# Performance work log

Measured on AMD Instinct MI355X. Metric: run time of the kernel, lower is better.

Reference implementation:

```python
import jax, jax.numpy as jnp
import numpy as np

N, L, P = 1024, 4096, 8192  # batch, simulated length, acquired spectrum length


def batch_linspace(a, b, n):
    # a, b: [..., 1] -> [..., n]
    t = jnp.arange(n, dtype=jnp.float32) / (n - 1)
    return a + (b - a) * t


def bounded_random_walk(start, end, std, lower, upper, noise):
    """Vectorized bounded random walk with reflecting bounds.
    start/end/std/lower/upper: [N]; noise: [N, L] uniform(0,1) steps."""
    n = noise.shape[-1]
    rand = jnp.cumsum(std[:, None] * (noise - 0.5), axis=-1)          # [N, L]
    rand_trend = batch_linspace(rand[:, :1], rand[:, -1:], n)
    deltas = rand - rand_trend                                         # detrended walk
    bounds = (upper - lower)[:, None]
    span = deltas.max(-1, keepdims=True) - deltas.min(-1, keepdims=True)
    deltas = deltas / jnp.maximum(1.0, span / bounds)                  # squeeze into bound width
    trend = batch_linspace(start[:, None], end[:, None], n)
    ub = upper[:, None] - trend
    lb = lower[:, None] - trend
    over = deltas - ub
    deltas = jnp.where(over >= 0, ub - over, deltas)                   # reflect off upper bound
    under = lb - deltas
    deltas = jnp.where(under >= 0, lb + under, deltas)                 # reflect off lower bound
    return trend + deltas


def batch_smooth(x, w):
    """Per-sample box-filter smoothing with zero ('constant') padding.
    x: [N, L] float; w: [N] int window sizes."""
    n, l = x.shape
    xp = jnp.pad(x, ((0, 0), (l, l)))
    cs = jnp.concatenate([jnp.zeros((n, 1), x.dtype), jnp.cumsum(xp, -1)], -1)
    t = jnp.arange(l)
    lo = t[None, :] - w[:, None] // 2 + l                              # [N, L]
    hi = lo + w[:, None]
    box = jnp.take_along_axis(cs, hi, 1) - jnp.take_along_axis(cs, lo, 1)
    return box / w[:, None].astype(x.dtype)


def normalize_max(x):
    denom = jnp.max(jnp.abs(x), axis=-1, keepdims=True)
    return x / jnp.where(denom == 0, 1.0, denom)


def sim2acquired(sig, ppm_lo, ppm_hi, ppm):
    """Map simulated signal on [ppm_lo, ppm_hi] grid onto full acquired ppm axis
    (linear interp, zero outside simulated range)."""
    l = sig.shape[-1]
    xs = jnp.linspace(ppm_lo, ppm_hi, l)
    return jax.vmap(lambda s: jnp.interp(ppm, xs, s, left=0.0, right=0.0))(sig)


def hilbert(x):
    """FFT-based analytic signal; returns stacked [N, 2, P] (real, imag)."""
    p = x.shape[-1]
    h = jnp.zeros(p, x.dtype).at[0].set(1.0).at[p // 2].set(1.0).at[1:p // 2].set(2.0)
    a = jnp.fft.ifft(jnp.fft.fft(x, axis=-1) * h, axis=-1)
    return jnp.stack([jnp.real(a), jnp.imag(a)], axis=1)


def setup_inputs() -> dict:
    key = jax.random.key(0)
    ks = jax.random.split(key, 10)
    u = lambda k, lo, hi: jax.random.uniform(k, (N,), minval=lo, maxval=hi, dtype=jnp.float32)
    start = u(ks[0], -1.0, 1.0)
    end = u(ks[1], -1.0, 1.0)
    std = u(ks[2], 0.05, 0.3)
    lower_bnd = u(ks[3], -2.0, -1.5)
    upper_bnd = u(ks[4], 1.5, 2.0)
    windows = jax.random.randint(ks[5], (N,), 8, 128, dtype=jnp.int32)
    scale = u(ks[6], 0.5, 2.0)
    noise = jax.random.uniform(ks[7], (N, L), dtype=jnp.float32)
    omit_mask = (jax.random.uniform(ks[8], (N,)) > 0.1).astype(jnp.float32)  # drop_prob=0.1
    ppm = jnp.linspace(-2.0, 10.0, P).astype(jnp.float32)                     # acquired ppm axis
    ppm_range = jnp.array([0.2, 4.2], jnp.float32)                            # simulated range
    return dict(start=start, end=end, std=std, lower_bnd=lower_bnd,
                upper_bnd=upper_bnd, windows=windows, scale=scale, noise=noise,
                omit_mask=omit_mask, ppm=ppm, ppm_range=ppm_range)


def reference(start, end, std, lower_bnd, upper_bnd, windows, scale, noise,
              omit_mask, ppm, ppm_range):
    walk = bounded_random_walk(start, end, std, lower_bnd, upper_bnd, noise)  # [N, L]
    b = batch_smooth(walk, windows)
    trend = batch_linspace(b[:, :1], b[:, -1:], b.shape[-1])
    b = normalize_max(b - trend)
    b = b * omit_mask[:, None]                                                # rand_omit
    acq = sim2acquired(b * scale[:, None], ppm_range[0], ppm_range[1], ppm)   # [N, P]
    raw = hilbert(acq)                                                        # [N, 2, P]
    return (jnp.flip(raw, axis=-1), raw)
```

## Files before the change

### kernel.cpp

```cpp
#include <hip/hip_runtime.h>

#define NB 1024
#define LL 4096
#define PP 8192
#define FN 4096

#define PIF 3.14159265358979323846f

__device__ __forceinline__ float2 cadd(float2 a, float2 b){ return make_float2(a.x+b.x, a.y+b.y); }
__device__ __forceinline__ float2 csub(float2 a, float2 b){ return make_float2(a.x-b.x, a.y-b.y); }
__device__ __forceinline__ float2 cmul(float2 a, float2 b){ return make_float2(a.x*b.x - a.y*b.y, a.x*b.y + a.y*b.x); }

__device__ __forceinline__ int SW(int p){ return p ^ ((p >> 4) & 15); }

__device__ __forceinline__ int rho(int k){
    return ((k & 3) << 10) | (((k >> 2) & 3) << 8) | (((k >> 4) & 3) << 6)
         | (((k >> 6) & 3) << 4) | (((k >> 8) & 3) << 2) | ((k >> 10) & 3);
}

template<int H>
__device__ __forceinline__ void fwd_r4(float2* buf, int tid){
#pragma unroll
    for (int m = 0; m < FN/4/256; m++){
        int b = tid + m*256;
        int j = b & (H-1);
        int i = ((b & ~(H-1)) << 2) | j;
        int a0 = SW(i), a1 = SW(i+H), a2 = SW(i+2*H), a3 = SW(i+3*H);
        float2 x0 = buf[a0], x1 = buf[a1], x2 = buf[a2], x3 = buf[a3];
        float2 t0 = cadd(x0,x2), t1 = cadd(x1,x3);
        float2 t2 = csub(x0,x2), t3 = csub(x1,x3);
        float2 y0 = cadd(t0,t1);
        float2 y2 = csub(t0,t1);
        float2 y1 = make_float2(t2.x + t3.y, t2.y - t3.x);
        float2 y3 = make_float2(t2.x - t3.y, t2.y + t3.x);
        if (H > 1){
            float sn, cn; __sincosf((-PIF/(2.0f*(float)H)) * (float)j, &sn, &cn);
            float2 E  = make_float2(cn, sn);
            float2 E2 = cmul(E,E);
            float2 E3 = cmul(E2,E);
            y1 = cmul(y1,E); y2 = cmul(y2,E2); y3 = cmul(y3,E3);
        }
        buf[a0] = y0; buf[a1] = y1; buf[a2] = y2; buf[a3] = y3;
    }
}

template<int H>
__device__ __forceinline__ void inv_r4(float2* buf, int tid){
#pragma unroll
    for (int m = 0; m < FN/4/256; m++){
        int b = tid + m*256;
        int j = b & (H-1);
        int i = ((b & ~(H-1)) << 2) | j;
        int a0 = SW(i), a1 = SW(i+H), a2 = SW(i+2*H), a3 = SW(i+3*H);
        float2 z0 = buf[a0], z1 = buf[a1], z2 = buf[a2], z3 = buf[a3];
        if (H > 1){
            float sn, cn; __sincosf((PIF/(2.0f*(float)H)) * (float)j, &sn, &cn);
            float2 E  = make_float2(cn, sn);
            float2 E2 = cmul(E,E);
            float2 E3 = cmul(E2,E);
            z1 = cmul(z1,E); z2 = cmul(z2,E2); z3 = cmul(z3,E3);
        }
        float2 s0 = cadd(z0,z2), s1 = cadd(z1,z3);
        float2 s2 = csub(z0,z2), s3 = csub(z1,z3);
        buf[a0] = cadd(s0,s1);
        buf[a2] = csub(s0,s1);
        buf[a1] = make_float2(s2.x - s3.y, s2.y + s3.x);
        buf[a3] = make_float2(s2.x + s3.y, s2.y - s3.x);
    }
}

__device__ __forceinline__ void hilbert_mid(float2* buf, int tid){
    const float s = 1.0f/(2.0f*(float)FN);
#pragma unroll
    for (int m = 0; m < 8; m++){
        int k = ((tid & 31) << 6) | ((tid >> 5) << 3) | m;
        if (k == 0){
            buf[0] = make_float2(0.0f, 0.0f);
            int p = SW(2);
            float2 Z = buf[p];
            buf[p] = make_float2(-2.0f*s*Z.y, 2.0f*s*Z.x);
        } else {
            int pk = SW(rho(k));
            int pj = SW(rho(FN - k));
            float2 Zk = buf[pk];
            float2 Zj = buf[pj];
            float ux = Zk.x + Zj.x, uy = Zk.y - Zj.y;
            float vx = Zk.x - Zj.x, vy = Zk.y + Zj.y;
            float sn, cn; __sincosf((PIF/(float)FN) * (float)k, &sn, &cn);
            float2 zk, zj;
            zk.x = s * ((ux*cn - uy*sn) - (vx*cn + vy*sn));
            zk.y = s * ((ux*sn + uy*cn) + (vx*sn - vy*cn));
            float u2x = ux,  u2y = -uy;
            float v2x = -vx, v2y = vy;
            zj.x = s * ((v2x*cn - v2y*sn) - (u2x*cn + u2y*sn));
            zj.y = s * ((v2x*sn + v2y*cn) + (u2x*sn - u2y*cn));
            buf[pk] = zk;
            buf[pj] = zj;
        }
    }
}

__global__ __launch_bounds__(256, 4) void k_all(
    const float* __restrict__ g_start,
    const float* __restrict__ g_end,
    const float* __restrict__ g_std,
    const float* __restrict__ g_low,
    const float* __restrict__ g_up,
    const int*   __restrict__ g_win,
    const float* __restrict__ g_scale,
    const float* __restrict__ g_noise,
    const float* __restrict__ g_omit,
    const float* __restrict__ g_ppm,
    const float* __restrict__ g_ppmr,
    float* __restrict__ g_out)
{
    __shared__ float2 buf[FN];
    float* bf  = (float*)buf;
#define CSI(t) ((t) + ((t) >> 5))
    float* cs  = bf;
    float* tmp = bf + 4226;
    float* shv = bf + 4234;

    const int n    = blockIdx.x;
    const int tid  = threadIdx.x;
    const int lane = tid & 63;
    const int wid  = tid >> 6;
    const float st = g_start[n];
    const float en = g_end[n];
    const float sd = g_std[n];
    const float lo = g_low[n];
    const float up = g_up[n];
    const int   w  = g_win[n];
    const float inv_nm1 = 1.0f / (float)(LL - 1);

    float v[16];
    {
        const float4* p = (const float4*)(g_noise + (size_t)n * LL) + (size_t)tid * 4;
#pragma unroll
        for (int q = 0; q < 4; q++) {
            float4 t4 = p[q];
            v[4*q+0] = t4.x; v[4*q+1] = t4.y; v[4*q+2] = t4.z; v[4*q+3] = t4.w;
        }
    }
#pragma unroll
    for (int k = 0; k < 16; k++) v[k] = sd * (v[k] - 0.5f);

    float run = 0.0f;
#pragma unroll
    for (int k = 0; k < 16; k++) { run += v[k]; v[k] = run; }
    float ws = run;
#pragma unroll
    for (int off = 1; off < 64; off <<= 1) { float t = __shfl_up(ws, off); if (lane >= off) ws += t; }
    if (lane == 63) tmp[wid] = ws;
    if (tid == 0)   shv[0] = v[0];
    __syncthreads();
    float w0 = tmp[0], w1 = tmp[1], w2s = tmp[2], w3 = tmp[3];
    const float rT = w0 + w1 + w2s + w3;
    const float r0 = shv[0];
    float base = (wid > 0 ? w0 : 0.0f) + (wid > 1 ? w1 : 0.0f) + (wid > 2 ? w2s : 0.0f);
    float excl = base + ws - run;
    __syncthreads();

    float del[16];
    float mx = -INFINITY, mn = INFINITY;
#pragma unroll
    for (int k = 0; k < 16; k++) {
        int t = tid * 16 + k;
        float d = (excl + v[k]) - (r0 + (rT - r0) * ((float)t * inv_nm1));
        del[k] = d;
        mx = fmaxf(mx, d); mn = fminf(mn, d);
    }
#pragma unroll
    for (int off = 32; off > 0; off >>= 1) {
        mx = fmaxf(mx, __shfl_xor(mx, off));
        mn = fminf(mn, __shfl_xor(mn, off));
    }
    if (lane == 0) { tmp[wid] = mx; tmp[4 + wid] = mn; }
    __syncthreads();
    mx = fmaxf(fmaxf(tmp[0], tmp[1]), fmaxf(tmp[2], tmp[3]));
    mn = fminf(fminf(tmp[4], tmp[5]), fminf(tmp[6], tmp[7]));
    __syncthreads();

    const float qs = fmaxf(1.0f, (mx - mn) / (up - lo));

    float wv[16];
#pragma unroll
    for (int k = 0; k < 16; k++) {
        int t = tid * 16 + k;
        float tr  = st + (en - st) * ((float)t * inv_nm1);
        float ub  = up - tr;
        float lb2 = lo - tr;
        float d = del[k] / qs;
        float over = d - ub;
        d = (over >= 0.0f) ? (ub - over) : d;
        float under = lb2 - d;
        d = (under >= 0.0f) ? (lb2 + under) : d;
        wv[k] = tr + d;
    }

    run = 0.0f;
#pragma unroll
    for (int k = 0; k < 16; k++) { run += wv[k]; wv[k] = run; }
    ws = run;
#pragma unroll
    for (int off = 1; off < 64; off <<= 1) { float t = __shfl_up(ws, off); if (lane >= off) ws += t; }
    if (lane == 63) tmp[wid] = ws;
    __syncthreads();
    w0 = tmp[0]; w1 = tmp[1]; w2s = tmp[2]; w3 = tmp[3];
    const float grand2 = w0 + w1 + w2s + w3;
    base = (wid > 0 ? w0 : 0.0f) + (wid > 1 ? w1 : 0.0f) + (wid > 2 ? w2s : 0.0f);
    float excl2 = base + ws - run;
#pragma unroll
    for (int k = 0; k < 16; k++) {
        int t = tid * 16 + k;
        cs[CSI(t)] = excl2 + ((k == 0) ? 0.0f : wv[k - 1]);
    }
    if (tid == 255) cs[CSI(LL)] = grand2;
    __syncthreads();

    const int wh = w / 2;
    const float invw = 1.0f / (float)w;
    float bvals[16];
#pragma unroll
    for (int k = 0; k < 16; k++) {
        int t  = tid + 256 * k;
        int li = t - wh;
        int hi = li + w;
        li = (li < 0) ? 0 : li;
        hi = (hi > LL) ? LL : hi;
        bvals[k] = (cs[CSI(hi)] - cs[CSI(li)]) * invw;
    }
    if (tid == 0)   shv[0] = bvals[0];
    if (tid == 255) shv[1] = bvals[15];
    __syncthreads();
    const float b0 = shv[0], bL = shv[1];

    float am = 0.0f;
#pragma unroll
    for (int k = 0; k < 16; k++) {
        int t = tid + 256 * k;
        bvals[k] -= b0 + (bL - b0) * ((float)t * inv_nm1);
        am = fmaxf(am, fabsf(bvals[k]));
    }
#pragma unroll
    for (int off = 32; off > 0; off >>= 1) am = fmaxf(am, __shfl_xor(am, off));
    if (lane == 0) tmp[wid] = am;
    __syncthreads();
    float denom = fmaxf(fmaxf(tmp[0], tmp[1]), fmaxf(tmp[2], tmp[3]));
    denom = (denom == 0.0f) ? 1.0f : denom;
    const float fac = g_omit[n] * g_scale[n] / denom;

#pragma unroll
    for (int k = 0; k < 16; k++) {
        int t = tid + 256 * k;
        bf[t] = bvals[k] * fac;
    }
    __syncthreads();

    const float xlo = g_ppmr[0];
    const float xhi = g_ppmr[1];
    const float posmul = (float)(LL - 1) / (xhi - xlo);
    float val[PP / 256];
#pragma unroll
    for (int m = 0; m < PP / 256; m++) {
        int jj = tid + m * 256;
        float x = g_ppm[jj];
        float re = 0.0f;
        if (x >= xlo && x <= xhi) {
            float pos = (x - xlo) * posmul;
            int idx = (int)floorf(pos);
            idx = (idx < 0) ? 0 : ((idx > LL - 2) ? (LL - 2) : idx);
            float fr = pos - (float)idx;
            float s0 = bf[idx], s1 = bf[idx + 1];
            re = s0 + (s1 - s0) * fr;
        }
        val[m] = re;
    }
    __syncthreads();

    const size_t base1 = (size_t)NB * 2 * PP + (size_t)n * 2 * PP;
    const size_t base0 = (size_t)n * 2 * PP;
#pragma unroll
    for (int m = 0; m < PP / 256; m++) {
        int jj = tid + m * 256;
        bf[2 * SW(jj >> 1) + (jj & 1)] = val[m];
        g_out[base1 + jj]            = val[m];
        g_out[base0 + (PP - 1 - jj)] = val[m];
    }
    __syncthreads();

    fwd_r4<1024>(buf, tid); __syncthreads();
    fwd_r4< 256>(buf, tid); __syncthreads();
    fwd_r4<  64>(buf, tid); __syncthreads();
    fwd_r4<  16>(buf, tid); __syncthreads();
    fwd_r4<   4>(buf, tid); __syncthreads();
    fwd_r4<   1>(buf, tid); __syncthreads();

    hilbert_mid(buf, tid); __syncthreads();

    inv_r4<   1>(buf, tid); __syncthreads();
    inv_r4<   4>(buf, tid); __syncthreads();
    inv_r4<  16>(buf, tid); __syncthreads();
    inv_r4<  64>(buf, tid); __syncthreads();
    inv_r4< 256>(buf, tid); __syncthreads();
    inv_r4<1024>(buf, tid); __syncthreads();

#pragma unroll
    for (int m = 0; m < FN / 256; m++) {
        int p = tid + m * 256;
        float2 a = buf[SW(p)];
        *(float2*)(g_out + base1 + PP + 2 * p)          = a;
        *(float2*)(g_out + base0 + 2 * PP - 2 - 2 * p)  = make_float2(a.y, a.x);
    }
}

extern "C" void kernel_launch(void* const* d_in, const int* in_sizes, int n_in,
                              void* d_out, int out_size, void* d_ws, size_t ws_size,
                              hipStream_t stream)
{
    const float* start = (const float*)d_in[0];
    const float* end_  = (const float*)d_in[1];
    const float* stdv  = (const float*)d_in[2];
    const float* lowb  = (const float*)d_in[3];
    const float* upb   = (const float*)d_in[4];
    const int*   win   = (const int*)d_in[5];
    const float* scl   = (const float*)d_in[6];
    const float* noise = (const float*)d_in[7];
    const float* omit  = (const float*)d_in[8];
    const float* ppm   = (const float*)d_in[9];
    const float* ppmr  = (const float*)d_in[10];
    float* out = (float*)d_out;

    hipLaunchKernelGGL(k_all, dim3(NB), dim3(256), 0, stream,
                       start, end_, stdv, lowb, upb, win, scl, noise, omit,
                       ppm, ppmr, out);
}
```

Before: 187.4 us.

## Fuse FFT radix-4 stages into register-resident radix-16 passes

Replaces the six-pass radix-4 shared-memory FFT (and its inverse) with three passes that each do two radix-4 stages on 16 values held in registers. Interpolation results feed the first pass directly from registers, and the last inverse pass writes straight to global memory. This removes several LDS round-trips and barriers per transform and uses vectorized float2 loads and stores for ppm and outputs. The cost is higher register pressure from the 16-element complex arrays, which may reduce occupancy.

```diff
diff --git a/kernel.cpp b/kernel.cpp
--- a/kernel.cpp
+++ b/kernel.cpp
@@ -18,55 +18,52 @@
          | (((k >> 6) & 3) << 4) | (((k >> 8) & 3) << 2) | ((k >> 10) & 3);
 }
 
-template<int H>
-__device__ __forceinline__ void fwd_r4(float2* buf, int tid){
-#pragma unroll
-    for (int m = 0; m < FN/4/256; m++){
-        int b = tid + m*256;
-        int j = b & (H-1);
-        int i = ((b & ~(H-1)) << 2) | j;
-        int a0 = SW(i), a1 = SW(i+H), a2 = SW(i+2*H), a3 = SW(i+3*H);
-        float2 x0 = buf[a0], x1 = buf[a1], x2 = buf[a2], x3 = buf[a3];
-        float2 t0 = cadd(x0,x2), t1 = cadd(x1,x3);
-        float2 t2 = csub(x0,x2), t3 = csub(x1,x3);
-        float2 y0 = cadd(t0,t1);
-        float2 y2 = csub(t0,t1);
-        float2 y1 = make_float2(t2.x + t3.y, t2.y - t3.x);
-        float2 y3 = make_float2(t2.x - t3.y, t2.y + t3.x);
-        if (H > 1){
-            float sn, cn; __sincosf((-PIF/(2.0f*(float)H)) * (float)j, &sn, &cn);
-            float2 E  = make_float2(cn, sn);
-            float2 E2 = cmul(E,E);
-            float2 E3 = cmul(E2,E);
-            y1 = cmul(y1,E); y2 = cmul(y2,E2); y3 = cmul(y3,E3);
-        }
-        buf[a0] = y0; buf[a1] = y1; buf[a2] = y2; buf[a3] = y3;
-    }
-}
-
-template<int H>
-__device__ __forceinline__ void inv_r4(float2* buf, int tid){
-#pragma unroll
-    for (int m = 0; m < FN/4/256; m++){
-        int b = tid + m*256;
-        int j = b & (H-1);
-        int i = ((b & ~(H-1)) << 2) | j;
-        int a0 = SW(i), a1 = SW(i+H), a2 = SW(i+2*H), a3 = SW(i+3*H);
-        float2 z0 = buf[a0], z1 = buf[a1], z2 = buf[a2], z3 = buf[a3];
-        if (H > 1){
-            float sn, cn; __sincosf((PIF/(2.0f*(float)H)) * (float)j, &sn, &cn);
-            float2 E  = make_float2(cn, sn);
-            float2 E2 = cmul(E,E);
-            float2 E3 = cmul(E2,E);
-            z1 = cmul(z1,E); z2 = cmul(z2,E2); z3 = cmul(z3,E3);
-        }
-        float2 s0 = cadd(z0,z2), s1 = cadd(z1,z3);
-        float2 s2 = csub(z0,z2), s3 = csub(z1,z3);
-        buf[a0] = cadd(s0,s1);
-        buf[a2] = csub(s0,s1);
-        buf[a1] = make_float2(s2.x - s3.y, s2.y + s3.x);
-        buf[a3] = make_float2(s2.x + s3.y, s2.y - s3.x);
-    }
+__device__ __forceinline__ float2 CFc(int a){
+    return (a==1) ? make_float2(0.92387953251f, -0.38268343236f)
+         : (a==2) ? make_float2(0.70710678119f, -0.70710678119f)
+         :          make_float2(0.38268343236f, -0.92387953251f);
+}
+__device__ __forceinline__ float2 CIc(int a){ float2 c = CFc(a); return make_float2(c.x, -c.y); }
+
+template<int S>
+__device__ __forceinline__ void bf4f(float2* x, float2 E){
+    float2 E2 = cmul(E,E), E3 = cmul(E2,E);
+    float2 t0 = cadd(x[0],x[2*S]), t1 = cadd(x[S],x[3*S]);
+    float2 t2 = csub(x[0],x[2*S]), t3 = csub(x[S],x[3*S]);
+    x[0]   = cadd(t0,t1);
+    x[2*S] = cmul(csub(t0,t1), E2);
+    x[S]   = cmul(make_float2(t2.x + t3.y, t2.y - t3.x), E);
+    x[3*S] = cmul(make_float2(t2.x - t3.y, t2.y + t3.x), E3);
+}
+template<int S>
+__device__ __forceinline__ void bf4f_nt(float2* x){
+    float2 t0 = cadd(x[0],x[2*S]), t1 = cadd(x[S],x[3*S]);
+    float2 t2 = csub(x[0],x[2*S]), t3 = csub(x[S],x[3*S]);
+    x[0]   = cadd(t0,t1);
+    x[2*S] = csub(t0,t1);
+    x[S]   = make_float2(t2.x + t3.y, t2.y - t3.x);
+    x[3*S] = make_float2(t2.x - t3.y, t2.y + t3.x);
+}
+template<int S>
+__device__ __forceinline__ void bf4i(float2* x, float2 E){
+    float2 E2 = cmul(E,E), E3 = cmul(E2,E);
+    float2 z0 = x[0], z1 = cmul(x[S],E), z2 = cmul(x[2*S],E2), z3 = cmul(x[3*S],E3);
+    float2 s0 = cadd(z0,z2), s1 = cadd(z1,z3);
+    float2 s2 = csub(z0,z2), s3 = csub(z1,z3);
+    x[0]   = cadd(s0,s1);
+    x[2*S] = csub(s0,s1);
+    x[S]   = make_float2(s2.x - s3.y, s2.y + s3.x);
+    x[3*S] = make_float2(s2.x + s3.y, s2.y - s3.x);
+}
+template<int S>
+__device__ __forceinline__ void bf4i_nt(float2* x){
+    float2 z0 = x[0], z1 = x[S], z2 = x[2*S], z3 = x[3*S];
+    float2 s0 = cadd(z0,z2), s1 = cadd(z1,z3);
+    float2 s2 = csub(z0,z2), s3 = csub(z1,z3);
+    x[0]   = cadd(s0,s1);
+    x[2*S] = csub(s0,s1);
+    x[S]   = make_float2(s2.x - s3.y, s2.y + s3.x);
+    x[3*S] = make_float2(s2.x + s3.y, s2.y - s3.x);
 }
 
 __device__ __forceinline__ void hilbert_mid(float2* buf, int tid){
@@ -260,57 +257,166 @@
     const float xlo = g_ppmr[0];
     const float xhi = g_ppmr[1];
     const float posmul = (float)(LL - 1) / (xhi - xlo);
-    float val[PP / 256];
-#pragma unroll
-    for (int m = 0; m < PP / 256; m++) {
-        int jj = tid + m * 256;
-        float x = g_ppm[jj];
-        float re = 0.0f;
-        if (x >= xlo && x <= xhi) {
-            float pos = (x - xlo) * posmul;
-            int idx = (int)floorf(pos);
-            idx = (idx < 0) ? 0 : ((idx > LL - 2) ? (LL - 2) : idx);
-            float fr = pos - (float)idx;
-            float s0 = bf[idx], s1 = bf[idx + 1];
-            re = s0 + (s1 - s0) * fr;
-        }
-        val[m] = re;
-    }
-    __syncthreads();
-
     const size_t base1 = (size_t)NB * 2 * PP + (size_t)n * 2 * PP;
     const size_t base0 = (size_t)n * 2 * PP;
-#pragma unroll
-    for (int m = 0; m < PP / 256; m++) {
-        int jj = tid + m * 256;
-        bf[2 * SW(jj >> 1) + (jj & 1)] = val[m];
-        g_out[base1 + jj]            = val[m];
-        g_out[base0 + (PP - 1 - jj)] = val[m];
-    }
-    __syncthreads();
-
-    fwd_r4<1024>(buf, tid); __syncthreads();
-    fwd_r4< 256>(buf, tid); __syncthreads();
-    fwd_r4<  64>(buf, tid); __syncthreads();
-    fwd_r4<  16>(buf, tid); __syncthreads();
-    fwd_r4<   4>(buf, tid); __syncthreads();
-    fwd_r4<   1>(buf, tid); __syncthreads();
-
-    hilbert_mid(buf, tid); __syncthreads();
-
-    inv_r4<   1>(buf, tid); __syncthreads();
-    inv_r4<   4>(buf, tid); __syncthreads();
-    inv_r4<  16>(buf, tid); __syncthreads();
-    inv_r4<  64>(buf, tid); __syncthreads();
-    inv_r4< 256>(buf, tid); __syncthreads();
-    inv_r4<1024>(buf, tid); __syncthreads();
-
-#pragma unroll
-    for (int m = 0; m < FN / 256; m++) {
-        int p = tid + m * 256;
-        float2 a = buf[SW(p)];
-        *(float2*)(g_out + base1 + PP + 2 * p)          = a;
-        *(float2*)(g_out + base0 + 2 * PP - 2 - 2 * p)  = make_float2(a.y, a.x);
+
+    auto interp1 = [&](float x) -> float {
+        if (x < xlo || x > xhi) return 0.0f;
+        float pos = (x - xlo) * posmul;
+        int idx = (int)floorf(pos);
+        idx = (idx < 0) ? 0 : ((idx > LL - 2) ? (LL - 2) : idx);
+        float fr = pos - (float)idx;
+        float s0 = bf[idx], s1 = bf[idx + 1];
+        return s0 + (s1 - s0) * fr;
+    };
+
+    float2 X[16];
+#pragma unroll
+    for (int b = 0; b < 4; b++)
+#pragma unroll
+    for (int a = 0; a < 4; a++) {
+        int p = tid + 256 * a + 1024 * b;
+        float2 pm = *(const float2*)(g_ppm + 2 * p);
+        float re0 = interp1(pm.x);
+        float re1 = interp1(pm.y);
+        X[a + 4 * b] = make_float2(re0, re1);
+        *(float2*)(g_out + base1 + 2 * p)          = make_float2(re0, re1);
+        *(float2*)(g_out + base0 + PP - 2 - 2 * p) = make_float2(re1, re0);
+    }
+    __syncthreads();
+
+    {
+        float sn, cn;
+        __sincosf((-PIF / 2048.0f) * (float)tid, &sn, &cn);
+        float2 Eb = make_float2(cn, sn);
+#pragma unroll
+        for (int a = 0; a < 4; a++) {
+            float2 E = (a == 0) ? Eb : cmul(Eb, CFc(a));
+            bf4f<4>(&X[a], E);
+        }
+        __sincosf((-PIF / 512.0f) * (float)tid, &sn, &cn);
+        float2 E = make_float2(cn, sn);
+#pragma unroll
+        for (int b = 0; b < 4; b++) bf4f<1>(&X[4 * b], E);
+#pragma unroll
+        for (int b = 0; b < 4; b++)
+#pragma unroll
+        for (int a = 0; a < 4; a++)
+            buf[SW(tid + 256 * a + 1024 * b)] = X[a + 4 * b];
+    }
+    __syncthreads();
+
+    const int u  = tid >> 4;
+    const int lw = tid & 15;
+    const int pb = u * 256 + lw;
+    {
+#pragma unroll
+        for (int b = 0; b < 4; b++)
+#pragma unroll
+        for (int a = 0; a < 4; a++)
+            X[a + 4 * b] = buf[SW(pb + 64 * b + 16 * a)];
+        float sn, cn;
+        __sincosf((-PIF / 128.0f) * (float)lw, &sn, &cn);
+        float2 Eb = make_float2(cn, sn);
+#pragma unroll
+        for (int a = 0; a < 4; a++) {
+            float2 E = (a == 0) ? Eb : cmul(Eb, CFc(a));
+            bf4f<4>(&X[a], E);
+        }
+        __sincosf((-PIF / 32.0f) * (float)lw, &sn, &cn);
+        float2 E = make_float2(cn, sn);
+#pragma unroll
+        for (int b = 0; b < 4; b++) bf4f<1>(&X[4 * b], E);
+#pragma unroll
+        for (int b = 0; b < 4; b++)
+#pragma unroll
+        for (int a = 0; a < 4; a++)
+            buf[SW(pb + 64 * b + 16 * a)] = X[a + 4 * b];
+    }
+    __syncthreads();
+
+    {
+#pragma unroll
+        for (int c = 0; c < 16; c++) X[c] = buf[SW(16 * tid + c)];
+        bf4f_nt<4>(&X[0]);
+#pragma unroll
+        for (int a = 1; a < 4; a++) bf4f<4>(&X[a], CFc(a));
+#pragma unroll
+        for (int b = 0; b < 4; b++) bf4f_nt<1>(&X[4 * b]);
+#pragma unroll
+        for (int c = 0; c < 16; c++) buf[SW(16 * tid + c)] = X[c];
+    }
+    __syncthreads();
+
+    hilbert_mid(buf, tid);
+    __syncthreads();
+
+    {
+#pragma unroll
+        for (int c = 0; c < 16; c++) X[c] = buf[SW(16 * tid + c)];
+#pragma unroll
+        for (int b = 0; b < 4; b++) bf4i_nt<1>(&X[4 * b]);
+        bf4i_nt<4>(&X[0]);
+#pragma unroll
+        for (int a = 1; a < 4; a++) bf4i<4>(&X[a], CIc(a));
+#pragma unroll
+        for (int c = 0; c < 16; c++) buf[SW(16 * tid + c)] = X[c];
+    }
+    __syncthreads();
+
+    {
+#pragma unroll
+        for (int b = 0; b < 4; b++)
+#pragma unroll
+        for (int a = 0; a < 4; a++)
+            X[a + 4 * b] = buf[SW(pb + 64 * b + 16 * a)];
+        float sn, cn;
+        __sincosf((PIF / 32.0f) * (float)lw, &sn, &cn);
+        float2 E = make_float2(cn, sn);
+#pragma unroll
+        for (int b = 0; b < 4; b++) bf4i<1>(&X[4 * b], E);
+        __sincosf((PIF / 128.0f) * (float)lw, &sn, &cn);
+        float2 Eb = make_float2(cn, sn);
+#pragma unroll
+        for (int a = 0; a < 4; a++) {
+            float2 Ea = (a == 0) ? Eb : cmul(Eb, CIc(a));
+            bf4i<4>(&X[a], Ea);
+        }
+#pragma unroll
+        for (int b = 0; b < 4; b++)
+#pragma unroll
+        for (int a = 0; a < 4; a++)
+            buf[SW(pb + 64 * b + 16 * a)] = X[a + 4 * b];
+    }
+    __syncthreads();
+
+    {
+#pragma unroll
+        for (int b = 0; b < 4; b++)
+#pragma unroll
+        for (int a = 0; a < 4; a++)
+            X[a + 4 * b] = buf[SW(tid + 256 * a + 1024 * b)];
+        float sn, cn;
+        __sincosf((PIF / 512.0f) * (float)tid, &sn, &cn);
+        float2 E = make_float2(cn, sn);
+#pragma unroll
+        for (int b = 0; b < 4; b++) bf4i<1>(&X[4 * b], E);
+        __sincosf((PIF / 2048.0f) * (float)tid, &sn, &cn);
+        float2 Eb = make_float2(cn, sn);
+#pragma unroll
+        for (int a = 0; a < 4; a++) {
+            float2 Ea = (a == 0) ? Eb : cmul(Eb, CIc(a));
+            bf4i<4>(&X[a], Ea);
+        }
+#pragma unroll
+        for (int b = 0; b < 4; b++)
+#pragma unroll
+        for (int a = 0; a < 4; a++) {
+            int p = tid + 256 * a + 1024 * b;
+            float2 vv = X[a + 4 * b];
+            *(float2*)(g_out + base1 + PP + 2 * p)         = vv;
+            *(float2*)(g_out + base0 + 2 * PP - 2 - 2 * p) = make_float2(vv.y, vv.x);
+        }
     }
 }
 
```

New measurement: 188.5 us. No clear change (+0.6%).

## Switch Hilbert FFT to radix-8 register stages with 512-thread blocks

Applied to the files above, without the earlier changes.

Replaces the six radix-4 shared-memory FFT passes (each way) with four radix-8 passes, where the first forward pass and last inverse pass run directly on register data. This removes one shared-memory round trip and a barrier per direction. Block size doubles to 512 threads with 8 elements per thread, and the padded shared layout changes from an XOR swizzle to a +2-per-16 pad. The interp and output stores are also vectorized as float2. Risks are higher register pressure and a larger shared footprint that may limit occupancy.

```diff
diff --git a/kernel.cpp b/kernel.cpp
--- a/kernel.cpp
+++ b/kernel.cpp
@@ -11,96 +11,46 @@
 __device__ __forceinline__ float2 csub(float2 a, float2 b){ return make_float2(a.x-b.x, a.y-b.y); }
 __device__ __forceinline__ float2 cmul(float2 a, float2 b){ return make_float2(a.x*b.x - a.y*b.y, a.x*b.y + a.y*b.x); }
 
-__device__ __forceinline__ int SW(int p){ return p ^ ((p >> 4) & 15); }
-
-__device__ __forceinline__ int rho(int k){
-    return ((k & 3) << 10) | (((k >> 2) & 3) << 8) | (((k >> 4) & 3) << 6)
-         | (((k >> 6) & 3) << 4) | (((k >> 8) & 3) << 2) | ((k >> 10) & 3);
+__device__ __forceinline__ int PH2(int p){ return p + 2*(p >> 4); }
+
+__device__ __forceinline__ int rev8(int k){
+    return ((k & 7) << 9) | (((k >> 3) & 7) << 6) | (((k >> 6) & 7) << 3) | ((k >> 9) & 7);
 }
 
-template<int H>
-__device__ __forceinline__ void fwd_r4(float2* buf, int tid){
-#pragma unroll
-    for (int m = 0; m < FN/4/256; m++){
-        int b = tid + m*256;
-        int j = b & (H-1);
-        int i = ((b & ~(H-1)) << 2) | j;
-        int a0 = SW(i), a1 = SW(i+H), a2 = SW(i+2*H), a3 = SW(i+3*H);
-        float2 x0 = buf[a0], x1 = buf[a1], x2 = buf[a2], x3 = buf[a3];
-        float2 t0 = cadd(x0,x2), t1 = cadd(x1,x3);
-        float2 t2 = csub(x0,x2), t3 = csub(x1,x3);
-        float2 y0 = cadd(t0,t1);
-        float2 y2 = csub(t0,t1);
-        float2 y1 = make_float2(t2.x + t3.y, t2.y - t3.x);
-        float2 y3 = make_float2(t2.x - t3.y, t2.y + t3.x);
-        if (H > 1){
-            float sn, cn; __sincosf((-PIF/(2.0f*(float)H)) * (float)j, &sn, &cn);
-            float2 E  = make_float2(cn, sn);
-            float2 E2 = cmul(E,E);
-            float2 E3 = cmul(E2,E);
-            y1 = cmul(y1,E); y2 = cmul(y2,E2); y3 = cmul(y3,E3);
-        }
-        buf[a0] = y0; buf[a1] = y1; buf[a2] = y2; buf[a3] = y3;
-    }
+__device__ __forceinline__ void core8f(float2* x){
+    const float c8 = 0.70710678118654752f;
+    float2 e0=cadd(x[0],x[4]), e1=cadd(x[1],x[5]), e2=cadd(x[2],x[6]), e3=cadd(x[3],x[7]);
+    float2 o0=csub(x[0],x[4]), o1=csub(x[1],x[5]), o2=csub(x[2],x[6]), o3=csub(x[3],x[7]);
+    float2 t1 = make_float2(c8*(o1.x + o1.y), c8*(o1.y - o1.x));
+    float2 t2 = make_float2(o2.y, -o2.x);
+    float2 t3 = make_float2(c8*(o3.y - o3.x), -c8*(o3.x + o3.y));
+    float2 a0=cadd(e0,e2), a1=cadd(e1,e3), a2=csub(e0,e2), a3=csub(e1,e3);
+    x[0]=cadd(a0,a1); x[4]=csub(a0,a1);
+    x[2]=make_float2(a2.x + a3.y, a2.y - a3.x);
+    x[6]=make_float2(a2.x - a3.y, a2.y + a3.x);
+    float2 b0=cadd(o0,t2), b1=cadd(t1,t3), b2=csub(o0,t2), b3=csub(t1,t3);
+    x[1]=cadd(b0,b1); x[5]=csub(b0,b1);
+    x[3]=make_float2(b2.x + b3.y, b2.y - b3.x);
+    x[7]=make_float2(b2.x - b3.y, b2.y + b3.x);
 }
-
-template<int H>
-__device__ __forceinline__ void inv_r4(float2* buf, int tid){
-#pragma unroll
-    for (int m = 0; m < FN/4/256; m++){
-        int b = tid + m*256;
-        int j = b & (H-1);
-        int i = ((b & ~(H-1)) << 2) | j;
-        int a0 = SW(i), a1 = SW(i+H), a2 = SW(i+2*H), a3 = SW(i+3*H);
-        float2 z0 = buf[a0], z1 = buf[a1], z2 = buf[a2], z3 = buf[a3];
-        if (H > 1){
-            float sn, cn; __sincosf((PIF/(2.0f*(float)H)) * (float)j, &sn, &cn);
-            float2 E  = make_float2(cn, sn);
-            float2 E2 = cmul(E,E);
-            float2 E3 = cmul(E2,E);
-            z1 = cmul(z1,E); z2 = cmul(z2,E2); z3 = cmul(z3,E3);
-        }
-        float2 s0 = cadd(z0,z2), s1 = cadd(z1,z3);
-        float2 s2 = csub(z0,z2), s3 = csub(z1,z3);
-        buf[a0] = cadd(s0,s1);
-        buf[a2] = csub(s0,s1);
-        buf[a1] = make_float2(s2.x - s3.y, s2.y + s3.x);
-        buf[a3] = make_float2(s2.x + s3.y, s2.y - s3.x);
-    }
+__device__ __forceinline__ void core8i(float2* x){
+    const float c8 = 0.70710678118654752f;
+    float2 e0=cadd(x[0],x[4]), e1=cadd(x[1],x[5]), e2=cadd(x[2],x[6]), e3=cadd(x[3],x[7]);
+    float2 o0=csub(x[0],x[4]), o1=csub(x[1],x[5]), o2=csub(x[2],x[6]), o3=csub(x[3],x[7]);
+    float2 t1 = make_float2(c8*(o1.x - o1.y), c8*(o1.y + o1.x));
+    float2 t2 = make_float2(-o2.y, o2.x);
+    float2 t3 = make_float2(-c8*(o3.x + o3.y), c8*(o3.x - o3.y));
+    float2 a0=cadd(e0,e2), a1=cadd(e1,e3), a2=csub(e0,e2), a3=csub(e1,e3);
+    x[0]=cadd(a0,a1); x[4]=csub(a0,a1);
+    x[2]=make_float2(a2.x - a3.y, a2.y + a3.x);
+    x[6]=make_float2(a2.x + a3.y, a2.y - a3.x);
+    float2 b0=cadd(o0,t2), b1=cadd(t1,t3), b2=csub(o0,t2), b3=csub(t1,t3);
+    x[1]=cadd(b0,b1); x[5]=csub(b0,b1);
+    x[3]=make_float2(b2.x - b3.y, b2.y + b3.x);
+    x[7]=make_float2(b2.x + b3.y, b2.y - b3.x);
 }
 
-__device__ __forceinline__ void hilbert_mid(float2* buf, int tid){
-    const float s = 1.0f/(2.0f*(float)FN);
-#pragma unroll
-    for (int m = 0; m < 8; m++){
-        int k = ((tid & 31) << 6) | ((tid >> 5) << 3) | m;
-        if (k == 0){
-            buf[0] = make_float2(0.0f, 0.0f);
-            int p = SW(2);
-            float2 Z = buf[p];
-            buf[p] = make_float2(-2.0f*s*Z.y, 2.0f*s*Z.x);
-        } else {
-            int pk = SW(rho(k));
-            int pj = SW(rho(FN - k));
-            float2 Zk = buf[pk];
-            float2 Zj = buf[pj];
-            float ux = Zk.x + Zj.x, uy = Zk.y - Zj.y;
-            float vx = Zk.x - Zj.x, vy = Zk.y + Zj.y;
-            float sn, cn; __sincosf((PIF/(float)FN) * (float)k, &sn, &cn);
-            float2 zk, zj;
-            zk.x = s * ((ux*cn - uy*sn) - (vx*cn + vy*sn));
-            zk.y = s * ((ux*sn + uy*cn) + (vx*sn - vy*cn));
-            float u2x = ux,  u2y = -uy;
-            float v2x = -vx, v2y = vy;
-            zj.x = s * ((v2x*cn - v2y*sn) - (u2x*cn + u2y*sn));
-            zj.y = s * ((v2x*sn + v2y*cn) + (u2x*sn - u2y*cn));
-            buf[pk] = zk;
-            buf[pj] = zj;
-        }
-    }
-}
-
-__global__ __launch_bounds__(256, 4) void k_all(
+__global__ __launch_bounds__(512, 6) void k_all(
     const float* __restrict__ g_start,
     const float* __restrict__ g_end,
     const float* __restrict__ g_std,
@@ -114,12 +64,12 @@
     const float* __restrict__ g_ppmr,
     float* __restrict__ g_out)
 {
-    __shared__ float2 buf[FN];
+    __shared__ alignas(16) float2 buf[4608];
     float* bf  = (float*)buf;
 #define CSI(t) ((t) + ((t) >> 5))
     float* cs  = bf;
     float* tmp = bf + 4226;
-    float* shv = bf + 4234;
+    float* shv = bf + 4242;
 
     const int n    = blockIdx.x;
     const int tid  = threadIdx.x;
@@ -133,41 +83,39 @@
     const int   w  = g_win[n];
     const float inv_nm1 = 1.0f / (float)(LL - 1);
 
-    float v[16];
-    {
-        const float4* p = (const float4*)(g_noise + (size_t)n * LL) + (size_t)tid * 4;
-#pragma unroll
-        for (int q = 0; q < 4; q++) {
-            float4 t4 = p[q];
-            v[4*q+0] = t4.x; v[4*q+1] = t4.y; v[4*q+2] = t4.z; v[4*q+3] = t4.w;
-        }
-    }
-#pragma unroll
-    for (int k = 0; k < 16; k++) v[k] = sd * (v[k] - 0.5f);
+    float r[8];
+    {
+        const float4* p = (const float4*)(g_noise + (size_t)n * LL) + (size_t)tid * 2;
+        float4 ta = p[0], tb = p[1];
+        r[0]=ta.x; r[1]=ta.y; r[2]=ta.z; r[3]=ta.w;
+        r[4]=tb.x; r[5]=tb.y; r[6]=tb.z; r[7]=tb.w;
+    }
+#pragma unroll
+    for (int k = 0; k < 8; k++) r[k] = sd * (r[k] - 0.5f);
 
     float run = 0.0f;
 #pragma unroll
-    for (int k = 0; k < 16; k++) { run += v[k]; v[k] = run; }
+    for (int k = 0; k < 8; k++) { run += r[k]; r[k] = run; }
     float ws = run;
 #pragma unroll
     for (int off = 1; off < 64; off <<= 1) { float t = __shfl_up(ws, off); if (lane >= off) ws += t; }
     if (lane == 63) tmp[wid] = ws;
-    if (tid == 0)   shv[0] = v[0];
-    __syncthreads();
-    float w0 = tmp[0], w1 = tmp[1], w2s = tmp[2], w3 = tmp[3];
-    const float rT = w0 + w1 + w2s + w3;
+    if (tid == 0)   shv[0] = r[0];
+    __syncthreads();
+    float t0=tmp[0],t1=tmp[1],t2=tmp[2],t3=tmp[3],t4=tmp[4],t5=tmp[5],t6=tmp[6],t7=tmp[7];
+    const float rT = ((t0+t1)+(t2+t3))+((t4+t5)+(t6+t7));
     const float r0 = shv[0];
-    float base = (wid > 0 ? w0 : 0.0f) + (wid > 1 ? w1 : 0.0f) + (wid > 2 ? w2s : 0.0f);
+    float base = (wid>0?t0:0.f)+(wid>1?t1:0.f)+(wid>2?t2:0.f)+(wid>3?t3:0.f)
+               + (wid>4?t4:0.f)+(wid>5?t5:0.f)+(wid>6?t6:0.f);
     float excl = base + ws - run;
     __syncthreads();
 
-    float del[16];
     float mx = -INFINITY, mn = INFINITY;
 #pragma unroll
-    for (int k = 0; k < 16; k++) {
-        int t = tid * 16 + k;
-        float d = (excl + v[k]) - (r0 + (rT - r0) * ((float)t * inv_nm1));
-        del[k] = d;
+    for (int k = 0; k < 8; k++) {
+        int t = tid * 8 + k;
+        float d = (excl + r[k]) - (r0 + (rT - r0) * ((float)t * inv_nm1));
+        r[k] = d;
         mx = fmaxf(mx, d); mn = fminf(mn, d);
     }
 #pragma unroll
@@ -175,142 +123,291 @@
         mx = fmaxf(mx, __shfl_xor(mx, off));
         mn = fminf(mn, __shfl_xor(mn, off));
     }
-    if (lane == 0) { tmp[wid] = mx; tmp[4 + wid] = mn; }
-    __syncthreads();
-    mx = fmaxf(fmaxf(tmp[0], tmp[1]), fmaxf(tmp[2], tmp[3]));
-    mn = fminf(fminf(tmp[4], tmp[5]), fminf(tmp[6], tmp[7]));
+    if (lane == 0) { tmp[wid] = mx; tmp[8 + wid] = mn; }
+    __syncthreads();
+    mx = fmaxf(fmaxf(fmaxf(tmp[0],tmp[1]),fmaxf(tmp[2],tmp[3])),
+               fmaxf(fmaxf(tmp[4],tmp[5]),fmaxf(tmp[6],tmp[7])));
+    mn = fminf(fminf(fminf(tmp[8],tmp[9]),fminf(tmp[10],tmp[11])),
+               fminf(fminf(tmp[12],tmp[13]),fminf(tmp[14],tmp[15])));
     __syncthreads();
 
     const float qs = fmaxf(1.0f, (mx - mn) / (up - lo));
 
-    float wv[16];
-#pragma unroll
-    for (int k = 0; k < 16; k++) {
-        int t = tid * 16 + k;
+#pragma unroll
+    for (int k = 0; k < 8; k++) {
+        int t = tid * 8 + k;
         float tr  = st + (en - st) * ((float)t * inv_nm1);
         float ub  = up - tr;
         float lb2 = lo - tr;
-        float d = del[k] / qs;
+        float d = r[k] / qs;
         float over = d - ub;
         d = (over >= 0.0f) ? (ub - over) : d;
         float under = lb2 - d;
         d = (under >= 0.0f) ? (lb2 + under) : d;
-        wv[k] = tr + d;
+        r[k] = tr + d;
     }
 
     run = 0.0f;
 #pragma unroll
-    for (int k = 0; k < 16; k++) { run += wv[k]; wv[k] = run; }
+    for (int k = 0; k < 8; k++) { run += r[k]; r[k] = run; }
     ws = run;
 #pragma unroll
     for (int off = 1; off < 64; off <<= 1) { float t = __shfl_up(ws, off); if (lane >= off) ws += t; }
     if (lane == 63) tmp[wid] = ws;
     __syncthreads();
-    w0 = tmp[0]; w1 = tmp[1]; w2s = tmp[2]; w3 = tmp[3];
-    const float grand2 = w0 + w1 + w2s + w3;
-    base = (wid > 0 ? w0 : 0.0f) + (wid > 1 ? w1 : 0.0f) + (wid > 2 ? w2s : 0.0f);
+    t0=tmp[0];t1=tmp[1];t2=tmp[2];t3=tmp[3];t4=tmp[4];t5=tmp[5];t6=tmp[6];t7=tmp[7];
+    const float grand2 = ((t0+t1)+(t2+t3))+((t4+t5)+(t6+t7));
+    base = (wid>0?t0:0.f)+(wid>1?t1:0.f)+(wid>2?t2:0.f)+(wid>3?t3:0.f)
+         + (wid>4?t4:0.f)+(wid>5?t5:0.f)+(wid>6?t6:0.f);
     float excl2 = base + ws - run;
 #pragma unroll
-    for (int k = 0; k < 16; k++) {
-        int t = tid * 16 + k;
-        cs[CSI(t)] = excl2 + ((k == 0) ? 0.0f : wv[k - 1]);
-    }
-    if (tid == 255) cs[CSI(LL)] = grand2;
+    for (int k = 0; k < 8; k++) {
+        int t = tid * 8 + k;
+        cs[CSI(t)] = excl2 + ((k == 0) ? 0.0f : r[k - 1]);
+    }
+    if (tid == 511) cs[CSI(LL)] = grand2;
     __syncthreads();
 
     const int wh = w / 2;
     const float invw = 1.0f / (float)w;
-    float bvals[16];
-#pragma unroll
-    for (int k = 0; k < 16; k++) {
-        int t  = tid + 256 * k;
+#pragma unroll
+    for (int k = 0; k < 8; k++) {
+        int t  = tid + 512 * k;
         int li = t - wh;
         int hi = li + w;
         li = (li < 0) ? 0 : li;
         hi = (hi > LL) ? LL : hi;
-        bvals[k] = (cs[CSI(hi)] - cs[CSI(li)]) * invw;
-    }
-    if (tid == 0)   shv[0] = bvals[0];
-    if (tid == 255) shv[1] = bvals[15];
+        r[k] = (cs[CSI(hi)] - cs[CSI(li)]) * invw;
+    }
+    if (tid == 0)   shv[0] = r[0];
+    if (tid == 511) shv[1] = r[7];
     __syncthreads();
     const float b0 = shv[0], bL = shv[1];
 
     float am = 0.0f;
 #pragma unroll
-    for (int k = 0; k < 16; k++) {
-        int t = tid + 256 * k;
-        bvals[k] -= b0 + (bL - b0) * ((float)t * inv_nm1);
-        am = fmaxf(am, fabsf(bvals[k]));
+    for (int k = 0; k < 8; k++) {
+        int t = tid + 512 * k;
+        r[k] -= b0 + (bL - b0) * ((float)t * inv_nm1);
+        am = fmaxf(am, fabsf(r[k]));
     }
 #pragma unroll
     for (int off = 32; off > 0; off >>= 1) am = fmaxf(am, __shfl_xor(am, off));
     if (lane == 0) tmp[wid] = am;
     __syncthreads();
-    float denom = fmaxf(fmaxf(tmp[0], tmp[1]), fmaxf(tmp[2], tmp[3]));
+    float denom = fmaxf(fmaxf(fmaxf(tmp[0],tmp[1]),fmaxf(tmp[2],tmp[3])),
+                        fmaxf(fmaxf(tmp[4],tmp[5]),fmaxf(tmp[6],tmp[7])));
     denom = (denom == 0.0f) ? 1.0f : denom;
     const float fac = g_omit[n] * g_scale[n] / denom;
-
-#pragma unroll
-    for (int k = 0; k < 16; k++) {
-        int t = tid + 256 * k;
-        bf[t] = bvals[k] * fac;
+    __syncthreads();
+
+#pragma unroll
+    for (int k = 0; k < 8; k++) {
+        int t = tid + 512 * k;
+        bf[t] = r[k] * fac;
     }
     __syncthreads();
 
     const float xlo = g_ppmr[0];
     const float xhi = g_ppmr[1];
     const float posmul = (float)(LL - 1) / (xhi - xlo);
-    float val[PP / 256];
-#pragma unroll
-    for (int m = 0; m < PP / 256; m++) {
-        int jj = tid + m * 256;
-        float x = g_ppm[jj];
-        float re = 0.0f;
-        if (x >= xlo && x <= xhi) {
-            float pos = (x - xlo) * posmul;
-            int idx = (int)floorf(pos);
-            idx = (idx < 0) ? 0 : ((idx > LL - 2) ? (LL - 2) : idx);
-            float fr = pos - (float)idx;
-            float s0 = bf[idx], s1 = bf[idx + 1];
-            re = s0 + (s1 - s0) * fr;
-        }
-        val[m] = re;
-    }
-    __syncthreads();
-
     const size_t base1 = (size_t)NB * 2 * PP + (size_t)n * 2 * PP;
     const size_t base0 = (size_t)n * 2 * PP;
-#pragma unroll
-    for (int m = 0; m < PP / 256; m++) {
-        int jj = tid + m * 256;
-        bf[2 * SW(jj >> 1) + (jj & 1)] = val[m];
-        g_out[base1 + jj]            = val[m];
-        g_out[base0 + (PP - 1 - jj)] = val[m];
-    }
-    __syncthreads();
-
-    fwd_r4<1024>(buf, tid); __syncthreads();
-    fwd_r4< 256>(buf, tid); __syncthreads();
-    fwd_r4<  64>(buf, tid); __syncthreads();
-    fwd_r4<  16>(buf, tid); __syncthreads();
-    fwd_r4<   4>(buf, tid); __syncthreads();
-    fwd_r4<   1>(buf, tid); __syncthreads();
-
-    hilbert_mid(buf, tid); __syncthreads();
-
-    inv_r4<   1>(buf, tid); __syncthreads();
-    inv_r4<   4>(buf, tid); __syncthreads();
-    inv_r4<  16>(buf, tid); __syncthreads();
-    inv_r4<  64>(buf, tid); __syncthreads();
-    inv_r4< 256>(buf, tid); __syncthreads();
-    inv_r4<1024>(buf, tid); __syncthreads();
-
-#pragma unroll
-    for (int m = 0; m < FN / 256; m++) {
-        int p = tid + m * 256;
-        float2 a = buf[SW(p)];
-        *(float2*)(g_out + base1 + PP + 2 * p)          = a;
-        *(float2*)(g_out + base0 + 2 * PP - 2 - 2 * p)  = make_float2(a.y, a.x);
+
+    auto interp1 = [&](float x) -> float {
+        if (x < xlo || x > xhi) return 0.0f;
+        float pos = (x - xlo) * posmul;
+        int idx = (int)floorf(pos);
+        idx = (idx < 0) ? 0 : ((idx > LL - 2) ? (LL - 2) : idx);
+        float fr = pos - (float)idx;
+        float s0 = bf[idx], s1 = bf[idx + 1];
+        return s0 + (s1 - s0) * fr;
+    };
+
+    float2 X[8];
+#pragma unroll
+    for (int m = 0; m < 8; m++) {
+        int p = tid + 512 * m;
+        float2 pm = *(const float2*)(g_ppm + 2 * p);
+        float re0 = interp1(pm.x);
+        float re1 = interp1(pm.y);
+        X[m] = make_float2(re0, re1);
+        *(float2*)(g_out + base1 + 2 * p)          = make_float2(re0, re1);
+        *(float2*)(g_out + base0 + PP - 2 - 2 * p) = make_float2(re1, re0);
+    }
+    __syncthreads();
+
+    const int bA = tid + 2 * (tid >> 4);
+    {
+        core8f(X);
+        float sn, cn; __sincosf((-PIF / 2048.0f) * (float)tid, &sn, &cn);
+        float2 E = make_float2(cn, sn), Er = E;
+        buf[bA]        = X[0];
+        buf[bA +  576] = cmul(X[1], Er); Er = cmul(Er, E);
+        buf[bA + 1152] = cmul(X[2], Er); Er = cmul(Er, E);
+        buf[bA + 1728] = cmul(X[3], Er); Er = cmul(Er, E);
+        buf[bA + 2304] = cmul(X[4], Er); Er = cmul(Er, E);
+        buf[bA + 2880] = cmul(X[5], Er); Er = cmul(Er, E);
+        buf[bA + 3456] = cmul(X[6], Er); Er = cmul(Er, E);
+        buf[bA + 4032] = cmul(X[7], Er);
+    }
+    __syncthreads();
+
+    const int j2 = tid & 63;
+    const int bB = (tid >> 6) * 576 + j2 + 2 * (j2 >> 4);
+    {
+#pragma unroll
+        for (int d = 0; d < 8; d++) X[d] = buf[bB + 72 * d];
+        core8f(X);
+        float sn, cn; __sincosf((-PIF / 256.0f) * (float)j2, &sn, &cn);
+        float2 E = make_float2(cn, sn), Er = E;
+        buf[bB]       = X[0];
+        buf[bB +  72] = cmul(X[1], Er); Er = cmul(Er, E);
+        buf[bB + 144] = cmul(X[2], Er); Er = cmul(Er, E);
+        buf[bB + 216] = cmul(X[3], Er); Er = cmul(Er, E);
+        buf[bB + 288] = cmul(X[4], Er); Er = cmul(Er, E);
+        buf[bB + 360] = cmul(X[5], Er); Er = cmul(Er, E);
+        buf[bB + 432] = cmul(X[6], Er); Er = cmul(Er, E);
+        buf[bB + 504] = cmul(X[7], Er);
+    }
+    __syncthreads();
+
+    const int j3 = tid & 7;
+    const int bC = (tid >> 3) * 72 + j3;
+    {
+        X[0]=buf[bC];    X[1]=buf[bC+8];  X[2]=buf[bC+18]; X[3]=buf[bC+26];
+        X[4]=buf[bC+36]; X[5]=buf[bC+44]; X[6]=buf[bC+54]; X[7]=buf[bC+62];
+        core8f(X);
+        float sn, cn; __sincosf((-PIF / 32.0f) * (float)j3, &sn, &cn);
+        float2 E = make_float2(cn, sn), Er = E;
+        buf[bC]    = X[0];
+        buf[bC+ 8] = cmul(X[1], Er); Er = cmul(Er, E);
+        buf[bC+18] = cmul(X[2], Er); Er = cmul(Er, E);
+        buf[bC+26] = cmul(X[3], Er); Er = cmul(Er, E);
+        buf[bC+36] = cmul(X[4], Er); Er = cmul(Er, E);
+        buf[bC+44] = cmul(X[5], Er); Er = cmul(Er, E);
+        buf[bC+54] = cmul(X[6], Er); Er = cmul(Er, E);
+        buf[bC+62] = cmul(X[7], Er);
+    }
+    __syncthreads();
+
+    const int f4 = 4 * tid + (tid >> 1);
+    float4* b4 = reinterpret_cast<float4*>(buf);
+    {
+        float4 a0 = b4[f4], a1 = b4[f4+1], a2 = b4[f4+2], a3 = b4[f4+3];
+        X[0]=make_float2(a0.x,a0.y); X[1]=make_float2(a0.z,a0.w);
+        X[2]=make_float2(a1.x,a1.y); X[3]=make_float2(a1.z,a1.w);
+        X[4]=make_float2(a2.x,a2.y); X[5]=make_float2(a2.z,a2.w);
+        X[6]=make_float2(a3.x,a3.y); X[7]=make_float2(a3.z,a3.w);
+        core8f(X);
+        b4[f4]   = make_float4(X[0].x,X[0].y,X[1].x,X[1].y);
+        b4[f4+1] = make_float4(X[2].x,X[2].y,X[3].x,X[3].y);
+        b4[f4+2] = make_float4(X[4].x,X[4].y,X[5].x,X[5].y);
+        b4[f4+3] = make_float4(X[6].x,X[6].y,X[7].x,X[7].y);
+    }
+    __syncthreads();
+
+    {
+        const float s = 1.0f / (2.0f * (float)FN);
+#pragma unroll
+        for (int m = 0; m < 4; m++) {
+            int k = ((tid & 31) << 6) | ((tid >> 5) << 2) | m;
+            if (k == 0) {
+                buf[0] = make_float2(0.0f, 0.0f);
+                float2 Z = buf[4];
+                buf[4] = make_float2(-2.0f*s*Z.y, 2.0f*s*Z.x);
+            } else {
+                int pk = PH2(rev8(k));
+                int pj = PH2(rev8(FN - k));
+                float2 Zk = buf[pk];
+                float2 Zj = buf[pj];
+                float ux = Zk.x + Zj.x, uy = Zk.y - Zj.y;
+                float vx = Zk.x - Zj.x, vy = Zk.y + Zj.y;
+                float sn, cn; __sincosf((PIF/(float)FN) * (float)k, &sn, &cn);
+                float2 zk, zj;
+                zk.x = s * ((ux*cn - uy*sn) - (vx*cn + vy*sn));
+                zk.y = s * ((ux*sn + uy*cn) + (vx*sn - vy*cn));
+                float u2x = ux,  u2y = -uy;
+                float v2x = -vx, v2y = vy;
+                zj.x = s * ((v2x*cn - v2y*sn) - (u2x*cn + u2y*sn));
+                zj.y = s * ((v2x*sn + v2y*cn) + (u2x*sn - u2y*cn));
+                buf[pk] = zk;
+                buf[pj] = zj;
+            }
+        }
+    }
+    __syncthreads();
+
+    {
+        float4 a0 = b4[f4], a1 = b4[f4+1], a2 = b4[f4+2], a3 = b4[f4+3];
+        X[0]=make_float2(a0.x,a0.y); X[1]=make_float2(a0.z,a0.w);
+        X[2]=make_float2(a1.x,a1.y); X[3]=make_float2(a1.z,a1.w);
+        X[4]=make_float2(a2.x,a2.y); X[5]=make_float2(a2.z,a2.w);
+        X[6]=make_float2(a3.x,a3.y); X[7]=make_float2(a3.z,a3.w);
+        core8i(X);
+        b4[f4]   = make_float4(X[0].x,X[0].y,X[1].x,X[1].y);
+        b4[f4+1] = make_float4(X[2].x,X[2].y,X[3].x,X[3].y);
+        b4[f4+2] = make_float4(X[4].x,X[4].y,X[5].x,X[5].y);
+        b4[f4+3] = make_float4(X[6].x,X[6].y,X[7].x,X[7].y);
+    }
+    __syncthreads();
+
+    {
+        X[0]=buf[bC];    X[1]=buf[bC+8];  X[2]=buf[bC+18]; X[3]=buf[bC+26];
+        X[4]=buf[bC+36]; X[5]=buf[bC+44]; X[6]=buf[bC+54]; X[7]=buf[bC+62];
+        float sn, cn; __sincosf((PIF / 32.0f) * (float)j3, &sn, &cn);
+        float2 E = make_float2(cn, sn), Er = E;
+        X[1]=cmul(X[1],Er); Er=cmul(Er,E);
+        X[2]=cmul(X[2],Er); Er=cmul(Er,E);
+        X[3]=cmul(X[3],Er); Er=cmul(Er,E);
+        X[4]=cmul(X[4],Er); Er=cmul(Er,E);
+        X[5]=cmul(X[5],Er); Er=cmul(Er,E);
+        X[6]=cmul(X[6],Er); Er=cmul(Er,E);
+        X[7]=cmul(X[7],Er);
+        core8i(X);
+        buf[bC]=X[0];    buf[bC+8]=X[1];  buf[bC+18]=X[2]; buf[bC+26]=X[3];
+        buf[bC+36]=X[4]; buf[bC+44]=X[5]; buf[bC+54]=X[6]; buf[bC+62]=X[7];
+    }
+    __syncthreads();
+
+    {
+#pragma unroll
+        for (int d = 0; d < 8; d++) X[d] = buf[bB + 72 * d];
+        float sn, cn; __sincosf((PIF / 256.0f) * (float)j2, &sn, &cn);
+        float2 E = make_float2(cn, sn), Er = E;
+        X[1]=cmul(X[1],Er); Er=cmul(Er,E);
+        X[2]=cmul(X[2],Er); Er=cmul(Er,E);
+        X[3]=cmul(X[3],Er); Er=cmul(Er,E);
+        X[4]=cmul(X[4],Er); Er=cmul(Er,E);
+        X[5]=cmul(X[5],Er); Er=cmul(Er,E);
+        X[6]=cmul(X[6],Er); Er=cmul(Er,E);
+        X[7]=cmul(X[7],Er);
+        core8i(X);
+#pragma unroll
+        for (int d = 0; d < 8; d++) buf[bB + 72 * d] = X[d];
+    }
+    __syncthreads();
+
+    {
+#pragma unroll
+        for (int d = 0; d < 8; d++) X[d] = buf[bA + 576 * d];
+        float sn, cn; __sincosf((PIF / 2048.0f) * (float)tid, &sn, &cn);
+        float2 E = make_float2(cn, sn), Er = E;
+        X[1]=cmul(X[1],Er); Er=cmul(Er,E);
+        X[2]=cmul(X[2],Er); Er=cmul(Er,E);
+        X[3]=cmul(X[3],Er); Er=cmul(Er,E);
+        X[4]=cmul(X[4],Er); Er=cmul(Er,E);
+        X[5]=cmul(X[5],Er); Er=cmul(Er,E);
+        X[6]=cmul(X[6],Er); Er=cmul(Er,E);
+        X[7]=cmul(X[7],Er);
+        core8i(X);
+#pragma unroll
+        for (int d = 0; d < 8; d++) {
+            int p = tid + 512 * d;
+            float2 vv = X[d];
+            *(float2*)(g_out + base1 + PP + 2 * p)         = vv;
+            *(float2*)(g_out + base0 + 2 * PP - 2 - 2 * p) = make_float2(vv.y, vv.x);
+        }
     }
 }
 
@@ -331,7 +428,7 @@
     const float* ppmr  = (const float*)d_in[10];
     float* out = (float*)d_out;
 
-    hipLaunchKernelGGL(k_all, dim3(NB), dim3(256), 0, stream,
+    hipLaunchKernelGGL(k_all, dim3(NB), dim3(512), 0, stream,
                        start, end_, stdv, lowb, upb, win, scl, noise, omit,
                        ppm, ppmr, out);
 }
```

New measurement: 176.0 us. -6.1%, faster.
